# Kernel tuning notes

Hardware: AMD Instinct MI355X
Metric: run time of the kernel (lower is better)

Reference implementation:

```python
import jax, jax.numpy as jnp
import numpy as np
import math

BIT = 8
N_HEAD = 12

def quantize_k(x, k=BIT):
    # DoReFa k-bit uniform quantizer with straight-through estimator
    n = float(2 ** k - 1)
    q = jnp.round(x * n) / n
    return x + jax.lax.stop_gradient(q - x)

def weight_quant(w, k=BIT):
    # DoReFa weight quantization: tanh normalize to [0,1], quantize, map back to [-1,1]
    t = jnp.tanh(w)
    t = t / (2.0 * jnp.max(jnp.abs(t))) + 0.5
    return 2.0 * quantize_k(t, k) - 1.0

def act_quant(x, k=BIT):
    # DoReFa activation quantization: clamp to [0,1] then k-bit quantize
    return quantize_k(jnp.clip(x, 0.0, 1.0), k)

def setup_inputs() -> dict:
    key = jax.random.key(0)
    k1, k2, k3 = jax.random.split(key, 3)
    B, S, NX = 8, 1024, 768
    x = jax.random.normal(k1, (B, S, NX), dtype=jnp.float32)
    W_attn = 0.02 * jax.random.normal(k2, (NX, 3 * NX), dtype=jnp.float32)
    b_attn = jnp.zeros((3 * NX,), dtype=jnp.float32)
    W_proj = 0.02 * jax.random.normal(k3, (NX, NX), dtype=jnp.float32)
    b_proj = jnp.zeros((NX,), dtype=jnp.float32)
    return {"x": x, "W_attn": W_attn, "b_attn": b_attn, "W_proj": W_proj, "b_proj": b_proj}

def reference(x, W_attn, b_attn, W_proj, b_proj):
    B, S, NX = x.shape
    H = N_HEAD
    hd = NX // H
    # quantized c_attn (Conv1D)
    qkv = jnp.einsum('bsn,nf->bsf', x, weight_quant(W_attn)) + b_attn  # [B,S,3*NX]
    q, k, v = jnp.split(qkv, 3, axis=-1)
    def split_heads(t):
        return t.reshape(B, S, H, hd).transpose(0, 2, 1, 3)  # [B,H,S,hd]
    q = act_quant(split_heads(q))
    k = act_quant(split_heads(k))
    v = act_quant(split_heads(v))
    # manual causal attention, scale=True
    w = jnp.einsum('bhqd,bhkd->bhqk', q, k) / math.sqrt(hd)  # [B,H,S,S]
    mask = jnp.tril(jnp.ones((S, S), dtype=x.dtype))
    w = w * mask - 10000.0 * (1.0 - mask)
    w = jax.nn.softmax(w, axis=-1)
    a = jnp.einsum('bhqk,bhkd->bhqd', w, v)  # [B,H,S,hd]
    a = a.transpose(0, 2, 1, 3).reshape(B, S, NX)  # merge heads
    a = jnp.einsum('bsn,nf->bsf', a, weight_quant(W_proj)) + b_proj
    # present = stack(key.transpose(-2,-1), value) -> both [B,H,S,hd]
    present = jnp.stack((k, v))
    return (a, present)
```

## Files before the change

### kernel.cpp

```cpp
#include <hip/hip_runtime.h>
#include <math.h>

#define B_   8
#define S_   1024
#define NXc  768
#define H_   12
#define HDc  64
#define M_   (B_*S_)
#define NQKV (3*NXc)

typedef __attribute__((ext_vector_type(8))) short short8;
typedef __attribute__((ext_vector_type(8))) _Float16 half8;
typedef __attribute__((ext_vector_type(4))) float f32x4;

__device__ inline unsigned short f2h(float f) {
  union { _Float16 h; unsigned short u; } c;
  c.h = (_Float16)f;
  return c.u;
}

__device__ inline void gl_lds16(const unsigned short* g, unsigned short* l) {
  __builtin_amdgcn_global_load_lds(
      (const __attribute__((address_space(1))) void*)g,
      (__attribute__((address_space(3))) void*)l, 16, 0, 0);
}

static const size_t UA_OFF_F  = 0;
static const size_t UA_F_CNT  = ((size_t)NQKV * NXc + 1) / 2;
static const size_t UP_OFF_F  = UA_OFF_F + UA_F_CNT;
static const size_t UP_F_CNT  = ((size_t)NXc * NXc + 1) / 2;
static const size_t QH_OFF_F  = UP_OFF_F + UP_F_CNT;
static const size_t HALF_CNT  = ((size_t)M_ * NXc + 1) / 2;
static const size_t KH_OFF_F  = QH_OFF_F + HALF_CNT;
static const size_t VHT_OFF_F = KH_OFF_F + HALF_CNT;
static const size_t AHF_OFF_F = VHT_OFF_F + HALF_CNT;
static const size_t SC_OFF    = AHF_OFF_F + HALF_CNT;
static const size_t WS_FLOATS_NEEDED = SC_OFF + 256;

__global__ __launch_bounds__(256) void k_prep(
    const float* __restrict__ x, unsigned short* __restrict__ xh,
    const float* __restrict__ wa, const float* __restrict__ wp,
    float* __restrict__ scp) {
  const int bid = blockIdx.x;
  if (bid < 3072) {
    int i = bid * 256 + threadIdx.x;
    const float* src = x + (size_t)i * 8;
    float4 f0 = *(const float4*)src;
    float4 f1 = *(const float4*)(src + 4);
    float fv[8] = {f0.x, f0.y, f0.z, f0.w, f1.x, f1.y, f1.z, f1.w};
    union { short8 v; unsigned short u[8]; } o;
#pragma unroll
    for (int j = 0; j < 8; ++j) o.u[j] = f2h(fv[j]);
    *(short8*)(xh + (size_t)i * 8) = o.v;
  } else {
    __shared__ float wpart[4];
    const int which = (bid - 3072) >> 7;
    const int xb = (bid - 3072) & 127;
    const float* w = which ? wp : wa;
    const int n = which ? (NXc * NXc) : (NXc * NQKV);
    float mx = 0.f;
    for (int i = xb * 256 + threadIdx.x; i < n; i += 128 * 256)
      mx = fmaxf(mx, fabsf(w[i]));
#pragma unroll
    for (int off = 32; off > 0; off >>= 1)
      mx = fmaxf(mx, __shfl_xor(mx, off));
    if ((threadIdx.x & 63) == 0) wpart[threadIdx.x >> 6] = mx;
    __syncthreads();
    if (threadIdx.x == 0)
      scp[which * 128 + xb] =
          fmaxf(fmaxf(wpart[0], wpart[1]), fmaxf(wpart[2], wpart[3]));
  }
}

__global__ __launch_bounds__(256) void k_quantw2(
    const float* __restrict__ wa, const float* __restrict__ wp,
    unsigned short* __restrict__ ua, unsigned short* __restrict__ up,
    const float* __restrict__ scp) {
  __shared__ unsigned short Ut[64][72];
  __shared__ float wred[4];
  const int bid = blockIdx.x;
  const int isp = (bid >= 432);
  const float* w = isp ? wp : wa;
  unsigned short* ut = isp ? up : ua;
  const int N = isp ? NXc : NQKV;
  const int K = NXc;
  const int idx = isp ? (bid - 432) : bid;
  const int nb = isp ? 12 : 36;
  const int bx = idx % nb, by = idx / nb;
  const int t = threadIdx.x;

  {
    float m = scp[isp * 128 + (t & 127)];
#pragma unroll
    for (int off = 32; off > 0; off >>= 1) m = fmaxf(m, __shfl_xor(m, off));
    if ((t & 63) == 0) wred[t >> 6] = m;
  }
  __syncthreads();
  const float gmax = fmaxf(fmaxf(wred[0], wred[1]), fmaxf(wred[2], wred[3]));
  const float inv2m = 0.5f / tanhf(gmax);

  const int k0 = by * 64, n0 = bx * 64;
  const int r = t >> 4, c4 = (t & 15) * 4;
#pragma unroll
  for (int rr = 0; rr < 4; ++rr) {
    int row = rr * 16 + r;
    float4 f = *(const float4*)(w + (size_t)(k0 + row) * N + n0 + c4);
    float fv[4] = {f.x, f.y, f.z, f.w};
#pragma unroll
    for (int j = 0; j < 4; ++j) {
      float tq = tanhf(fv[j]) * inv2m + 0.5f;
      float u = 2.0f * rintf(tq * 255.0f) - 255.0f;
      Ut[c4 + j][row] = f2h(u);
    }
  }
  __syncthreads();
#pragma unroll
  for (int rep = 0; rep < 2; ++rep) {
    int c = t + rep * 256;
    int n = c >> 3, slot = c & 7;
    short8 v = *(const short8*)&Ut[n][slot * 8];
    *(short8*)(ut + (size_t)(n0 + n) * K + k0 + slot * 8) = v;
  }
}

__global__ __launch_bounds__(256, 2) void k_gemm_qkv(
    const unsigned short* __restrict__ xh, const unsigned short* __restrict__ ua,
    const float* __restrict__ bias,
    unsigned short* __restrict__ qh, unsigned short* __restrict__ kh,
    unsigned short* __restrict__ vht, float* __restrict__ kq, float* __restrict__ vq) {
  __shared__ __align__(16) unsigned short SMEM[3 * 12288];
  unsigned short* Ahb3 = SMEM;
  unsigned short* Bsb3 = SMEM + 3 * 4096;
  unsigned short* T    = SMEM;

  const int bid = blockIdx.x;
  const int swz = (bid & 7) * 72 + (bid >> 3);
  const int bm = swz / 9, bn = swz % 9;
  const int part = bn / 3;

  const int t = threadIdx.x;
  const int w = t >> 6, lane = t & 63;
  const int wm = w >> 1, wn = w & 1;
  const int g = lane >> 4, ln = lane & 15;

  const unsigned short* Ab = xh + (size_t)bm * 128 * NXc;
  const unsigned short* Bb = ua + (size_t)bn * 256 * NXc;

  const int srow = t >> 2;
  const int aco  = (((t & 3) ^ ((t >> 3) & 3)) << 3);
  const int rsw  = ((g ^ ((ln >> 1) & 3)) << 3);

  f32x4 acc[4][8];
#pragma unroll
  for (int i = 0; i < 4; ++i)
#pragma unroll
    for (int j = 0; j < 8; ++j) acc[i][j] = (f32x4)(0.f);

  auto STAGE = [&](int tk, int buf) {
    const int k0 = tk * 32;
    unsigned short* Ah = Ahb3 + buf * 4096;
    unsigned short* Bs = Bsb3 + buf * 8192;
    gl_lds16(Ab + (size_t)srow * NXc + k0 + aco, &Ah[t * 8]);
    gl_lds16(Ab + (size_t)(srow + 64) * NXc + k0 + aco, &Ah[(256 + t) * 8]);
#pragma unroll
    for (int rr = 0; rr < 4; ++rr)
      gl_lds16(Bb + (size_t)(srow + rr * 64) * NXc + k0 + aco, &Bs[(rr * 256 + t) * 8]);
  };
  auto COMPUTE = [&](int buf) {
    const unsigned short* Ah = Ahb3 + buf * 4096;
    const unsigned short* Bs = Bsb3 + buf * 8192;
    half8 bfrag[8];
#pragma unroll
    for (int nf = 0; nf < 8; ++nf)
      bfrag[nf] = *(const half8*)&Bs[(wn * 128 + nf * 16 + ln) * 32 + rsw];
#pragma unroll
    for (int mf = 0; mf < 4; ++mf) {
      half8 ah = *(const half8*)&Ah[(wm * 64 + mf * 16 + ln) * 32 + rsw];
#pragma unroll
      for (int nf = 0; nf < 8; ++nf)
        acc[mf][nf] = __builtin_amdgcn_mfma_f32_16x16x32_f16(ah, bfrag[nf], acc[mf][nf], 0, 0, 0);
    }
  };

  STAGE(0, 0);
  STAGE(1, 1);
  for (int tk = 0; tk < 22; ++tk) {
    asm volatile("s_waitcnt vmcnt(6)" ::: "memory");
    __builtin_amdgcn_s_barrier();
    STAGE(tk + 2, (tk + 2) % 3);
    COMPUTE(tk % 3);
  }
  asm volatile("s_waitcnt vmcnt(6)" ::: "memory");
  __builtin_amdgcn_s_barrier();
  COMPUTE(22 % 3);
  asm volatile("s_waitcnt vmcnt(0)" ::: "memory");
  __builtin_amdgcn_s_barrier();
  COMPUTE(23 % 3);

  const float inv255 = 1.0f / 255.0f;
  if (part == 2) {
    __syncthreads();
#pragma unroll
    for (int mf = 0; mf < 4; ++mf) {
      int row0 = bm * 128 + wm * 64 + mf * 16 + g * 4;
#pragma unroll
      for (int nf = 0; nf < 8; ++nf) {
        int c = wn * 128 + nf * 16 + ln;
        int col = bn * 256 + c;
        float bv255 = bias[col] * 255.0f;
        int ff = col - 2 * NXc;
        int h = ff >> 6, d = ff & 63;
#pragma unroll
        for (int r = 0; r < 4; ++r) {
          float y255 = rintf(fminf(fmaxf(acc[mf][nf][r] + bv255, 0.f), 255.f));
          int row = row0 + r;
          int b = row >> 10, s = row & 1023;
          vq[(((size_t)b * H_ + h) * S_ + s) * HDc + d] = y255 * inv255;
          int sl = wm * 64 + mf * 16 + g * 4 + r;
          T[c * 136 + sl] = f2h(y255);
        }
      }
    }
    __syncthreads();
    const int bB = bm >> 3;
    const int s0 = (bm & 7) * 128;
    const int h0 = (bn - 6) * 4;
#pragma unroll
    for (int rep = 0; rep < 16; ++rep) {
      int idx = rep * 256 + t;
      int c = idx >> 4, sc2 = idx & 15;
      short8 v = *(const short8*)&T[c * 136 + sc2 * 8];
      int h = h0 + (c >> 6), d = c & 63;
      *(short8*)(vht + (((size_t)bB * H_ + h) * HDc + d) * S_ + s0 + sc2 * 8) = v;
    }
  } else {
    __syncthreads();
#pragma unroll
    for (int mf = 0; mf < 4; ++mf) {
      int lrow0 = wm * 64 + mf * 16 + g * 4;
#pragma unroll
      for (int nf = 0; nf < 8; ++nf) {
        int lcol = wn * 128 + nf * 16 + ln;
        float bv255 = bias[bn * 256 + lcol] * 255.0f;
#pragma unroll
        for (int r = 0; r < 4; ++r) {
          float y255 = rintf(fminf(fmaxf(acc[mf][nf][r] + bv255, 0.f), 255.f));
          T[(lrow0 + r) * 264 + lcol] = f2h(y255);
        }
      }
    }
    __syncthreads();
#pragma unroll
    for (int rep = 0; rep < 16; ++rep) {
      int idx = rep * 256 + t;
      int row = idx >> 5, cc = idx & 31;
      short8 v = *(const short8*)&T[row * 264 + cc * 8];
      int grow = bm * 128 + row;
      int b = grow >> 10, s = grow & 1023;
      int col = bn * 256 + cc * 8;
      int ff = col - part * NXc;
      int h = ff >> 6, d0 = ff & 63;
      size_t dst = (((size_t)b * H_ + h) * S_ + s) * HDc + d0;
      if (part == 0) {
        *(short8*)(qh + dst) = v;
      } else {
        *(short8*)(kh + dst) = v;
        union { short8 s8; half8 h8; } cvt; cvt.s8 = v;
        float4 f0, f1;
        f0.x = (float)cvt.h8[0] * inv255; f0.y = (float)cvt.h8[1] * inv255;
        f0.z = (float)cvt.h8[2] * inv255; f0.w = (float)cvt.h8[3] * inv255;
        f1.x = (float)cvt.h8[4] * inv255; f1.y = (float)cvt.h8[5] * inv255;
        f1.z = (float)cvt.h8[6] * inv255; f1.w = (float)cvt.h8[7] * inv255;
        *(float4*)(kq + dst) = f0;
        *(float4*)(kq + dst + 4) = f1;
      }
    }
  }
}

__global__ __launch_bounds__(256, 4) void k_gemm_proj(
    const unsigned short* __restrict__ ahf, const unsigned short* __restrict__ up,
    const float* __restrict__ bias, float* __restrict__ Cout) {
  __shared__ __align__(16) unsigned short SMEM[3 * (2048 + 4096)];
  unsigned short* Ahb3 = SMEM;
  unsigned short* Bsb3 = SMEM + 3 * 2048;

  const int bid = blockIdx.x;
  const int swz = (bid & 7) * 96 + (bid >> 3);
  const int bm = swz / 6, bn = swz % 6;

  const int t = threadIdx.x;
  const int w = t >> 6, lane = t & 63;
  const int wm = w >> 1, wn = w & 1;
  const int g = lane >> 4, ln = lane & 15;

  const unsigned short* Ab = ahf + (size_t)bm * 64 * NXc;
  const unsigned short* Bb = up + (size_t)bn * 128 * NXc;

  const int srow = t >> 2;
  const int aco  = (((t & 3) ^ ((t >> 3) & 3)) << 3);
  const int rsw  = ((g ^ ((ln >> 1) & 3)) << 3);

  f32x4 acc[2][4];
#pragma unroll
  for (int i = 0; i < 2; ++i)
#pragma unroll
    for (int j = 0; j < 4; ++j) acc[i][j] = (f32x4)(0.f);

  auto STAGE = [&](int tk, int buf) {
    const int k0 = tk * 32;
    unsigned short* Ah = Ahb3 + buf * 2048;
    unsigned short* Bs = Bsb3 + buf * 4096;
    gl_lds16(Ab + (size_t)srow * NXc + k0 + aco, &Ah[t * 8]);
    gl_lds16(Bb + (size_t)srow * NXc + k0 + aco, &Bs[t * 8]);
    gl_lds16(Bb + (size_t)(srow + 64) * NXc + k0 + aco, &Bs[(256 + t) * 8]);
  };
  auto COMPUTE = [&](int buf) {
    const unsigned short* Ah = Ahb3 + buf * 2048;
    const unsigned short* Bs = Bsb3 + buf * 4096;
    half8 bfrag[4];
#pragma unroll
    for (int nf = 0; nf < 4; ++nf)
      bfrag[nf] = *(const half8*)&Bs[(wn * 64 + nf * 16 + ln) * 32 + rsw];
#pragma unroll
    for (int mf = 0; mf < 2; ++mf) {
      half8 ah = *(const half8*)&Ah[(wm * 32 + mf * 16 + ln) * 32 + rsw];
#pragma unroll
      for (int nf = 0; nf < 4; ++nf)
        acc[mf][nf] = __builtin_amdgcn_mfma_f32_16x16x32_f16(ah, bfrag[nf], acc[mf][nf], 0, 0, 0);
    }
  };

  STAGE(0, 0);
  STAGE(1, 1);
  for (int tk = 0; tk < 22; ++tk) {
    asm volatile("s_waitcnt vmcnt(3)" ::: "memory");
    __builtin_amdgcn_s_barrier();
    __builtin_amdgcn_sched_barrier(0);
    STAGE(tk + 2, (tk + 2) % 3);
    COMPUTE(tk % 3);
  }
  asm volatile("s_waitcnt vmcnt(3)" ::: "memory");
  __builtin_amdgcn_s_barrier();
  __builtin_amdgcn_sched_barrier(0);
  COMPUTE(22 % 3);
  asm volatile("s_waitcnt vmcnt(0)" ::: "memory");
  __builtin_amdgcn_s_barrier();
  __builtin_amdgcn_sched_barrier(0);
  COMPUTE(23 % 3);

  const float inv255 = 1.0f / 255.0f;
#pragma unroll
  for (int mf = 0; mf < 2; ++mf) {
    int row0 = bm * 64 + wm * 32 + mf * 16 + g * 4;
#pragma unroll
    for (int nf = 0; nf < 4; ++nf) {
      int col = bn * 128 + wn * 64 + nf * 16 + ln;
      float bv = bias[col];
#pragma unroll
      for (int r = 0; r < 4; ++r)
        Cout[(size_t)(row0 + r) * NXc + col] = acc[mf][nf][r] * inv255 + bv;
    }
  }
}

__global__ __launch_bounds__(256, 4) void k_attn_pair(
    const unsigned short* __restrict__ qh, const unsigned short* __restrict__ kh,
    const unsigned short* __restrict__ vht, unsigned short* __restrict__ ahf) {
  __shared__ __align__(16) unsigned short Ks[2][64 * 64];
  __shared__ __align__(16) unsigned short Vt[2][64 * 64];
  __shared__ __align__(16) unsigned short Pp[4 * 16 * 64];

  const int bid = blockIdx.x;
  const int gidx = (bid & 7) * 96 + (bid >> 3);
  const int hid = gidx >> 3;
  const int p = gidx & 7;
  const int b = hid / H_, h = hid - b * H_;

  const size_t hoff = (size_t)hid * S_ * HDc;
  const unsigned short* qhp = qh + hoff;
  const unsigned short* khp = kh + hoff;
  const unsigned short* vhp = vht + hoff;

  const int t = threadIdx.x;
  const int w = t >> 6, lane = t & 63;
  const int g = lane >> 4, ln = lane & 15;

  const int r0 = t >> 3, c0 = (((t & 7) ^ (r0 & 7)) << 3);
  const int r1 = 32 + (t >> 3), c1 = (((t & 7) ^ (r1 & 7)) << 3);

  auto STAGE = [&](int jb, int buf) {
    gl_lds16(khp + (size_t)(jb * 64 + r0) * HDc + c0, &Ks[buf][t * 8]);
    gl_lds16(khp + (size_t)(jb * 64 + r1) * HDc + c1, &Ks[buf][(256 + t) * 8]);
    gl_lds16(vhp + (size_t)r0 * S_ + jb * 64 + c0, &Vt[buf][t * 8]);
    gl_lds16(vhp + (size_t)r1 * S_ + jb * 64 + c1, &Vt[buf][(256 + t) * 8]);
  };

  const float SCALE = 1.0f / (255.0f * 255.0f * 8.0f);

  int iq = p;
  half8 qfrag[2];
  {
    const unsigned short* qr = qhp + (size_t)(iq * 64 + w * 16 + ln) * HDc;
    qfrag[0] = *(const half8*)(qr + g * 8);
    qfrag[1] = *(const half8*)(qr + 32 + g * 8);
  }

  float l[4];
  f32x4 accO[4];
#pragma unroll
  for (int r = 0; r < 4; ++r) l[r] = 0.f;
#pragma unroll
  for (int nf = 0; nf < 4; ++nf) accO[nf] = (f32x4)(0.f);

  auto WRITEOUT = [&]() {
#pragma unroll
    for (int off = 1; off < 16; off <<= 1)
#pragma unroll
      for (int r = 0; r < 4; ++r) l[r] += __shfl_xor(l[r], off);
#pragma unroll
    for (int r = 0; r < 4; ++r) {
      float inv = 1.0f / (255.0f * l[r]);
      size_t row = (size_t)b * S_ + iq * 64 + w * 16 + g * 4 + r;
#pragma unroll
      for (int nf = 0; nf < 4; ++nf)
        ahf[row * NXc + h * HDc + nf * 16 + ln] = f2h(accO[nf][r] * inv);
    }
  };

  STAGE(0, 0);
  int jb = 0;
  for (int i = 0; i < 17; ++i) {
    const int buf = i & 1;
    __syncthreads();
    if (i + 1 < 17) {
      int njb = (i + 1 <= p) ? (i + 1) : (i - p);
      STAGE(njb, buf ^ 1);
    }

    f32x4 accS[4];
#pragma unroll
    for (int nf = 0; nf < 4; ++nf) accS[nf] = (f32x4)(0.f);
    __builtin_amdgcn_s_setprio(1);
#pragma unroll
    for (int ks = 0; ks < 2; ++ks)
#pragma unroll
      for (int nf = 0; nf < 4; ++nf) {
        int kvr = nf * 16 + ln;
        half8 bk = *(const half8*)&Ks[buf][kvr * 64 + ((ks * 32 + g * 8) ^ ((kvr & 7) << 3))];
        accS[nf] = __builtin_amdgcn_mfma_f32_16x16x32_f16(qfrag[ks], bk, accS[nf], 0, 0, 0);
      }
    __builtin_amdgcn_s_setprio(0);

    float pr[4][4];
    if (jb == iq) {
      const int grow = iq * 64 + w * 16 + g * 4;
      const int gcol = jb * 64 + ln;
#pragma unroll
      for (int nf = 0; nf < 4; ++nf)
#pragma unroll
        for (int r = 0; r < 4; ++r) {
          float pv = (gcol + nf * 16 > grow + r) ? 0.f : __expf(accS[nf][r] * SCALE);
          pr[nf][r] = pv;
          l[r] += pv;
        }
    } else {
#pragma unroll
      for (int nf = 0; nf < 4; ++nf)
#pragma unroll
        for (int r = 0; r < 4; ++r) {
          float pv = __expf(accS[nf][r] * SCALE);
          pr[nf][r] = pv;
          l[r] += pv;
        }
    }

#pragma unroll
    for (int nf = 0; nf < 4; ++nf)
#pragma unroll
      for (int r = 0; r < 4; ++r) {
        int prow = g * 4 + r;
        Pp[w * 1024 + prow * 64 + ((nf * 16 + ln) ^ ((prow & 7) << 3))] = f2h(pr[nf][r]);
      }

    __builtin_amdgcn_s_setprio(1);
#pragma unroll
    for (int ks = 0; ks < 2; ++ks) {
      half8 pa = *(const half8*)&Pp[w * 1024 + ln * 64 + ((ks * 32 + g * 8) ^ ((ln & 7) << 3))];
#pragma unroll
      for (int nf = 0; nf < 4; ++nf) {
        int d = nf * 16 + ln;
        half8 bv = *(const half8*)&Vt[buf][d * 64 + ((ks * 32 + g * 8) ^ ((d & 7) << 3))];
        accO[nf] = __builtin_amdgcn_mfma_f32_16x16x32_f16(pa, bv, accO[nf], 0, 0, 0);
      }
    }
    __builtin_amdgcn_s_setprio(0);

    if (i == p) {
      WRITEOUT();
#pragma unroll
      for (int r = 0; r < 4; ++r) l[r] = 0.f;
#pragma unroll
      for (int nf = 0; nf < 4; ++nf) accO[nf] = (f32x4)(0.f);
      iq = 15 - p;
      const unsigned short* qr2 = qhp + (size_t)(iq * 64 + w * 16 + ln) * HDc;
      qfrag[0] = *(const half8*)(qr2 + g * 8);
      qfrag[1] = *(const half8*)(qr2 + 32 + g * 8);
    } else if (i == 16) {
      WRITEOUT();
    }
    jb = (i + 1 <= p) ? (i + 1) : (i - p);
  }
}

extern "C" void kernel_launch(void* const* d_in, const int* in_sizes, int n_in,
                              void* d_out, int out_size, void* d_ws, size_t ws_size,
                              hipStream_t stream) {
  const float* x      = (const float*)d_in[0];
  const float* W_attn = (const float*)d_in[1];
  const float* b_attn = (const float*)d_in[2];
  const float* W_proj = (const float*)d_in[3];
  const float* b_proj = (const float*)d_in[4];

  float* out = (float*)d_out;
  float* ws  = (float*)d_ws;
  if (ws_size < WS_FLOATS_NEEDED * sizeof(float)) return;

  float* a_out = out;
  float* k_out = out + (size_t)M_ * NXc;
  float* v_out = k_out + (size_t)M_ * NXc;

  unsigned short* ua  = (unsigned short*)(ws + UA_OFF_F);
  unsigned short* up  = (unsigned short*)(ws + UP_OFF_F);
  unsigned short* qh  = (unsigned short*)(ws + QH_OFF_F);
  unsigned short* kh  = (unsigned short*)(ws + KH_OFF_F);
  unsigned short* vht = (unsigned short*)(ws + VHT_OFF_F);
  unsigned short* ahf = (unsigned short*)(ws + AHF_OFF_F);
  float* scp = ws + SC_OFF;

  unsigned short* xh = ahf;

  k_prep<<<3328, 256, 0, stream>>>(x, xh, W_attn, W_proj, scp);

  k_quantw2<<<576, 256, 0, stream>>>(W_attn, W_proj, ua, up, scp);

  k_gemm_qkv<<<(NQKV / 256) * (M_ / 128), 256, 0, stream>>>(
      xh, ua, b_attn, qh, kh, vht, k_out, v_out);

  k_attn_pair<<<768, 256, 0, stream>>>(qh, kh, vht, ahf);

  k_gemm_proj<<<(NXc / 128) * (M_ / 64), 256, 0, stream>>>(ahf, up, b_proj, a_out);
}
```

Before: 118.2 us.

## Replace paired causal query tiles with one query tile per block

The attention kernel used to give each block two query tiles (p and 15-p) so every block did the same 17 KV iterations. Now each block takes a single query tile, the grid doubles to 1536 blocks, and heavy tiles are scheduled first through the reversed iq index. This drops the mid-loop writeout and Q reload and adds more parallelism, at the cost of uneven per-block work and more blocks to schedule.

```diff
diff --git a/kernel.cpp b/kernel.cpp
--- a/kernel.cpp
+++ b/kernel.cpp
@@ -364,7 +364,7 @@
   }
 }
 
-__global__ __launch_bounds__(256, 4) void k_attn_pair(
+__global__ __launch_bounds__(256, 4) void k_attn_one(
     const unsigned short* __restrict__ qh, const unsigned short* __restrict__ kh,
     const unsigned short* __restrict__ vht, unsigned short* __restrict__ ahf) {
   __shared__ __align__(16) unsigned short Ks[2][64 * 64];
@@ -372,9 +372,9 @@
   __shared__ __align__(16) unsigned short Pp[4 * 16 * 64];
 
   const int bid = blockIdx.x;
-  const int gidx = (bid & 7) * 96 + (bid >> 3);
-  const int hid = gidx >> 3;
-  const int p = gidx & 7;
+  const int gidx = (bid & 7) * 192 + (bid >> 3);
+  const int hid = gidx >> 4;
+  const int iq = 15 - (gidx & 15);
   const int b = hid / H_, h = hid - b * H_;
 
   const size_t hoff = (size_t)hid * S_ * HDc;
@@ -398,7 +398,6 @@
 
   const float SCALE = 1.0f / (255.0f * 255.0f * 8.0f);
 
-  int iq = p;
   half8 qfrag[2];
   {
     const unsigned short* qr = qhp + (size_t)(iq * 64 + w * 16 + ln) * HDc;
@@ -413,30 +412,11 @@
 #pragma unroll
   for (int nf = 0; nf < 4; ++nf) accO[nf] = (f32x4)(0.f);
 
-  auto WRITEOUT = [&]() {
-#pragma unroll
-    for (int off = 1; off < 16; off <<= 1)
-#pragma unroll
-      for (int r = 0; r < 4; ++r) l[r] += __shfl_xor(l[r], off);
-#pragma unroll
-    for (int r = 0; r < 4; ++r) {
-      float inv = 1.0f / (255.0f * l[r]);
-      size_t row = (size_t)b * S_ + iq * 64 + w * 16 + g * 4 + r;
-#pragma unroll
-      for (int nf = 0; nf < 4; ++nf)
-        ahf[row * NXc + h * HDc + nf * 16 + ln] = f2h(accO[nf][r] * inv);
-    }
-  };
-
   STAGE(0, 0);
-  int jb = 0;
-  for (int i = 0; i < 17; ++i) {
+  for (int i = 0; i <= iq; ++i) {
     const int buf = i & 1;
     __syncthreads();
-    if (i + 1 < 17) {
-      int njb = (i + 1 <= p) ? (i + 1) : (i - p);
-      STAGE(njb, buf ^ 1);
-    }
+    if (i < iq) STAGE(i + 1, buf ^ 1);
 
     f32x4 accS[4];
 #pragma unroll
@@ -453,9 +433,9 @@
     __builtin_amdgcn_s_setprio(0);
 
     float pr[4][4];
-    if (jb == iq) {
+    if (i == iq) {
       const int grow = iq * 64 + w * 16 + g * 4;
-      const int gcol = jb * 64 + ln;
+      const int gcol = i * 64 + ln;
 #pragma unroll
       for (int nf = 0; nf < 4; ++nf)
 #pragma unroll
@@ -495,21 +475,19 @@
       }
     }
     __builtin_amdgcn_s_setprio(0);
-
-    if (i == p) {
-      WRITEOUT();
-#pragma unroll
-      for (int r = 0; r < 4; ++r) l[r] = 0.f;
-#pragma unroll
-      for (int nf = 0; nf < 4; ++nf) accO[nf] = (f32x4)(0.f);
-      iq = 15 - p;
-      const unsigned short* qr2 = qhp + (size_t)(iq * 64 + w * 16 + ln) * HDc;
-      qfrag[0] = *(const half8*)(qr2 + g * 8);
-      qfrag[1] = *(const half8*)(qr2 + 32 + g * 8);
-    } else if (i == 16) {
-      WRITEOUT();
-    }
-    jb = (i + 1 <= p) ? (i + 1) : (i - p);
+  }
+
+#pragma unroll
+  for (int off = 1; off < 16; off <<= 1)
+#pragma unroll
+    for (int r = 0; r < 4; ++r) l[r] += __shfl_xor(l[r], off);
+#pragma unroll
+  for (int r = 0; r < 4; ++r) {
+    float inv = 1.0f / (255.0f * l[r]);
+    size_t row = (size_t)b * S_ + iq * 64 + w * 16 + g * 4 + r;
+#pragma unroll
+    for (int nf = 0; nf < 4; ++nf)
+      ahf[row * NXc + h * HDc + nf * 16 + ln] = f2h(accO[nf][r] * inv);
   }
 }
 
@@ -547,7 +525,7 @@
   k_gemm_qkv<<<(NQKV / 256) * (M_ / 128), 256, 0, stream>>>(
       xh, ua, b_attn, qh, kh, vht, k_out, v_out);
 
-  k_attn_pair<<<768, 256, 0, stream>>>(qh, kh, vht, ahf);
+  k_attn_one<<<1536, 256, 0, stream>>>(qh, kh, vht, ahf);
 
   k_gemm_proj<<<(NXc / 128) * (M_ / 64), 256, 0, stream>>>(ahf, up, b_proj, a_out);
 }
```

Result: slower. 125.5 us (+6.2%).
